# Kernel tuning notes

Measured on AMD Instinct MI355X. Metric: run time of the kernel, lower is better.

## Reference

```python
import jax, jax.numpy as jnp
import numpy as np

DIM = 2048
DIM_HEAD = 64
HEADS = 16
FF_MULT = 4
LORA_R = 8
ATTN_INNER = DIM_HEAD * HEADS            # 1024
FF_INNER = DIM * FF_MULT                 # 8192
FUSED_DIMS = (ATTN_INNER, DIM_HEAD, DIM_HEAD, FF_INNER * 2)
B, N = 2, 2048


def setup_inputs() -> dict:
    key = jax.random.key(0)
    ks = jax.random.split(key, 12)
    s = 0.02
    inp = {
        "x": jax.random.normal(ks[0], (B, N, DIM), dtype=jnp.float32),
        "gamma": jnp.ones((DIM,), dtype=jnp.float32),
        "w_fused": jax.random.normal(ks[1], (DIM, sum(FUSED_DIMS)), dtype=jnp.float32) * s,
        "w_attn_out": jax.random.normal(ks[2], (ATTN_INNER, DIM), dtype=jnp.float32) * s,
        "w_ff_out": jax.random.normal(ks[3], (FF_INNER, DIM), dtype=jnp.float32) * s,
        "lora_q_a": jax.random.normal(ks[4], (DIM, LORA_R), dtype=jnp.float32) * s,
        "lora_q_b": jax.random.normal(ks[5], (LORA_R, ATTN_INNER), dtype=jnp.float32) * s,
        "lora_k_a": jax.random.normal(ks[6], (DIM, LORA_R), dtype=jnp.float32) * s,
        "lora_k_b": jax.random.normal(ks[7], (LORA_R, DIM_HEAD), dtype=jnp.float32) * s,
        "lora_v_a": jax.random.normal(ks[8], (DIM, LORA_R), dtype=jnp.float32) * s,
        "lora_v_b": jax.random.normal(ks[9], (LORA_R, DIM_HEAD), dtype=jnp.float32) * s,
        "lora_o_a": jax.random.normal(ks[10], (ATTN_INNER, LORA_R), dtype=jnp.float32) * s,
        "lora_o_b": jax.random.normal(ks[11], (LORA_R, DIM), dtype=jnp.float32) * s,
    }
    return inp


def _rotate_half(x):
    x1, x2 = jnp.split(x, 2, axis=-1)
    return jnp.concatenate((-x2, x1), axis=-1)


def _rope(pos, t):
    return t * jnp.cos(pos) + _rotate_half(t) * jnp.sin(pos)


def _forward(x, gamma, w_fused, w_attn_out, w_ff_out,
             lora_q_a, lora_q_b, lora_k_a, lora_k_b,
             lora_v_a, lora_v_b, lora_o_a, lora_o_b):
    b, n, d = x.shape
    # LayerNorm (beta = 0)
    mu = jnp.mean(x, axis=-1, keepdims=True)
    var = jnp.var(x, axis=-1, keepdims=True)
    xn = (x - mu) * jax.lax.rsqrt(var + 1e-5) * gamma

    fused = xn @ w_fused
    i0, i1, i2 = np.cumsum(FUSED_DIMS)[:3]
    q, k, v, ff = fused[..., :i0], fused[..., i0:i1], fused[..., i1:i2], fused[..., i2:]

    # LoRA additive terms
    q = q + (xn @ lora_q_a) @ lora_q_b
    k = k + (xn @ lora_k_a) @ lora_k_b
    v = v + (xn @ lora_v_a) @ lora_v_b

    q = q.reshape(b, n, HEADS, DIM_HEAD).transpose(0, 2, 1, 3)  # b h n d
    q = q * (DIM_HEAD ** -0.5)

    # rotary embedding: pos (n, dim_head)
    inv_freq = 1.0 / (10000.0 ** (jnp.arange(0, DIM_HEAD, 2, dtype=jnp.float32) / DIM_HEAD))
    freqs = jnp.arange(n, dtype=jnp.float32)[:, None] * inv_freq[None, :]
    pos = jnp.concatenate((freqs, freqs), axis=-1)
    q = _rope(pos, q)
    k = _rope(pos, k)  # k is b n d (multi-query, single kv head)

    sim = jnp.einsum('bhid,bjd->bhij', q, k)
    causal = jnp.triu(jnp.ones((n, n), dtype=bool), k=1)
    sim = jnp.where(causal, -jnp.finfo(sim.dtype).max, sim)
    attn = jax.nn.softmax(sim, axis=-1)
    out = jnp.einsum('bhij,bjd->bhid', attn, v)
    out = out.transpose(0, 2, 1, 3).reshape(b, n, ATTN_INNER)

    attn_out = out @ w_attn_out + (out @ lora_o_a) @ lora_o_b

    # SwiGLU: chunk -> (x_ff, gate); silu(gate) * x_ff
    x_ff, gate = jnp.split(ff, 2, axis=-1)
    ff_out = (jax.nn.silu(gate) * x_ff) @ w_ff_out

    return attn_out + ff_out


def reference(x, gamma, w_fused, w_attn_out, w_ff_out,
              lora_q_a, lora_q_b, lora_k_a, lora_k_b,
              lora_v_a, lora_v_b, lora_o_a, lora_o_b):
    return _forward(x, gamma, w_fused, w_attn_out, w_ff_out,
                    lora_q_a, lora_q_b, lora_k_a, lora_k_b,
                    lora_v_a, lora_v_b, lora_o_a, lora_o_b)
```

## Files before the change

### kernel.cpp

```cpp
#include <hip/hip_runtime.h>
#include <cstdint>


typedef __bf16 bf16_t;
typedef __bf16 bf16x8 __attribute__((ext_vector_type(8)));
typedef float f32x4 __attribute__((ext_vector_type(4)));

#define LOG2E 1.44269504088896340736f
#define LOG2_10K 13.287712379549449f

#define WAITCNT_VM(N) __builtin_amdgcn_s_waitcnt(0x0F70 | (N))

__device__ __forceinline__ void gload_lds16(const void* g, void* l) {
  __builtin_amdgcn_global_load_lds(
      (__attribute__((address_space(1))) void*)(uintptr_t)g,
      (__attribute__((address_space(3))) void*)(uint32_t)(uintptr_t)l,
      16, 0, 0);
}

__device__ __forceinline__ f32x4 mfma16(bf16x8 a, bf16x8 b, f32x4 c) {
  return __builtin_amdgcn_mfma_f32_16x16x32_bf16(a, b, c, 0, 0, 0);
}

__global__ __launch_bounds__(256) void ln_kernel(
    const float* __restrict__ x, const float* __restrict__ gamma,
    bf16_t* __restrict__ xn)
{
  const int row = blockIdx.x;
  const int t = threadIdx.x;
  const float4* xr = (const float4*)(x + (size_t)row * 2048);
  float4 a = xr[t * 2];
  float4 b = xr[t * 2 + 1];
  float s  = a.x + a.y + a.z + a.w + b.x + b.y + b.z + b.w;
  float ss = a.x*a.x + a.y*a.y + a.z*a.z + a.w*a.w
           + b.x*b.x + b.y*b.y + b.z*b.z + b.w*b.w;
  #pragma unroll
  for (int m = 1; m < 64; m <<= 1) {
    s  += __shfl_xor(s, m);
    ss += __shfl_xor(ss, m);
  }
  __shared__ float red[8];
  const int wave = t >> 6, lane = t & 63;
  if (lane == 0) { red[wave] = s; red[4 + wave] = ss; }
  __syncthreads();
  const float stot  = red[0] + red[1] + red[2] + red[3];
  const float sstot = red[4] + red[5] + red[6] + red[7];
  const float mu  = stot * (1.f / 2048.f);
  const float var = sstot * (1.f / 2048.f) - mu * mu;
  const float rs  = rsqrtf(var + 1e-5f);
  float v[8] = {a.x, a.y, a.z, a.w, b.x, b.y, b.z, b.w};
  bf16x8 o;
  #pragma unroll
  for (int e = 0; e < 8; ++e)
    o[e] = (bf16_t)((v[e] - mu) * rs * gamma[t * 8 + e]);
  *(bf16x8*)(xn + (size_t)row * 2048 + t * 8) = o;
}

__global__ __launch_bounds__(256) void transpose_wf_kernel(
    const float* __restrict__ w,
    const float* __restrict__ qa, const float* __restrict__ qb,
    const float* __restrict__ ka, const float* __restrict__ kb,
    const float* __restrict__ va, const float* __restrict__ vb,
    bf16_t* __restrict__ wfT)
{
  __shared__ float tile[64][65];
  const int t  = threadIdx.x;
  const int n0 = blockIdx.x * 64;
  const int k0 = blockIdx.y * 64;
  #pragma unroll
  for (int it = 0; it < 4; ++it) {
    const int kr = (t >> 4) + it * 16;
    const float4 vv = *(const float4*)(w + (size_t)(k0 + kr) * 17536 + n0 + (t & 15) * 4);
    tile[kr][(t & 15) * 4 + 0] = vv.x;
    tile[kr][(t & 15) * 4 + 1] = vv.y;
    tile[kr][(t & 15) * 4 + 2] = vv.z;
    tile[kr][(t & 15) * 4 + 3] = vv.w;
  }
  __syncthreads();
  const float* la = nullptr; const float* lb = nullptr;
  int nbo = 0, ldlb = 0;
  if (n0 < 1024)      { la = qa; lb = qb; nbo = n0;        ldlb = 1024; }
  else if (n0 < 1088) { la = ka; lb = kb; nbo = n0 - 1024; ldlb = 64;   }
  else if (n0 < 1152) { la = va; lb = vb; nbo = n0 - 1088; ldlb = 64;   }
  #pragma unroll
  for (int it = 0; it < 2; ++it) {
    const int nl = (t >> 3) + it * 32;
    const int kl = (t & 7) * 8;
    float vals[8];
    #pragma unroll
    for (int e = 0; e < 8; ++e) vals[e] = tile[kl + e][nl];
    if (la) {
      float bc[8];
      #pragma unroll
      for (int r = 0; r < 8; ++r) bc[r] = lb[r * ldlb + nbo + nl];
      #pragma unroll
      for (int e = 0; e < 8; ++e) {
        const float* ar = la + (size_t)(k0 + kl + e) * 8;
        float d = 0.f;
        #pragma unroll
        for (int r = 0; r < 8; ++r) d += ar[r] * bc[r];
        vals[e] += d;
      }
    }
    bf16x8 o;
    #pragma unroll
    for (int e = 0; e < 8; ++e) o[e] = (bf16_t)vals[e];
    *(bf16x8*)(wfT + (size_t)(n0 + nl) * 2048 + k0 + kl) = o;
  }
}

__global__ __launch_bounds__(256) void transpose_w2_kernel(
    const float* __restrict__ wff,
    const float* __restrict__ watt,
    const float* __restrict__ oa, const float* __restrict__ ob,
    bf16_t* __restrict__ w2T)
{
  __shared__ float tile[64][65];
  const int t  = threadIdx.x;
  const int n0 = blockIdx.x * 64;
  const int k0 = blockIdx.y * 64;
  const bool isatt = (k0 >= 8192);
  const float* src = isatt ? (watt + (size_t)(k0 - 8192) * 2048)
                           : (wff + (size_t)k0 * 2048);
  #pragma unroll
  for (int it = 0; it < 4; ++it) {
    const int kr = (t >> 4) + it * 16;
    const float4 vv = *(const float4*)(src + (size_t)kr * 2048 + n0 + (t & 15) * 4);
    tile[kr][(t & 15) * 4 + 0] = vv.x;
    tile[kr][(t & 15) * 4 + 1] = vv.y;
    tile[kr][(t & 15) * 4 + 2] = vv.z;
    tile[kr][(t & 15) * 4 + 3] = vv.w;
  }
  __syncthreads();
  #pragma unroll
  for (int it = 0; it < 2; ++it) {
    const int nl = (t >> 3) + it * 32;
    const int kl = (t & 7) * 8;
    float vals[8];
    #pragma unroll
    for (int e = 0; e < 8; ++e) vals[e] = tile[kl + e][nl];
    if (isatt) {
      float bc[8];
      #pragma unroll
      for (int r = 0; r < 8; ++r) bc[r] = ob[r * 2048 + n0 + nl];
      #pragma unroll
      for (int e = 0; e < 8; ++e) {
        const float* ar = oa + (size_t)(k0 - 8192 + kl + e) * 8;
        float d = 0.f;
        #pragma unroll
        for (int r = 0; r < 8; ++r) d += ar[r] * bc[r];
        vals[e] += d;
      }
    }
    bf16x8 o;
    #pragma unroll
    for (int e = 0; e < 8; ++e) o[e] = (bf16_t)vals[e];
    *(bf16x8*)(w2T + (size_t)(n0 + nl) * 9216 + k0 + kl) = o;
  }
}

__device__ __forceinline__ void gemm_core_128x128(
    const bf16_t* __restrict__ A, int ldA, int m0,
    const bf16_t* __restrict__ BT, int ldB, int n0,
    int K, bf16_t* As, bf16_t* Bs, f32x4* acc)
{
  const int t = threadIdx.x;
  const int wave = t >> 6;
  const int lane = t & 63;
  const int quad = lane >> 4;
  const int ln15 = lane & 15;
  const int wm = wave & 1, wn = wave >> 1;

  const bf16_t* gA = A + (size_t)(m0 + (t >> 2)) * ldA + ((t & 3) << 3);
  const bf16_t* gB = BT + (size_t)(n0 + (t >> 2)) * ldB + ((t & 3) << 3);
  char* lA = (char*)As + wave * 1024;
  char* lB = (char*)Bs + wave * 1024;
  const size_t sA64 = (size_t)64 * ldA;
  const size_t sB64 = (size_t)64 * ldB;
  const int aoff = (wm * 64 + ln15) * 32 + quad * 8;
  const int boff = (wn * 64 + ln15) * 32 + quad * 8;

  for (int kt = 0; kt < K; kt += 32) {
    gload_lds16(gA,        lA);
    gload_lds16(gA + sA64, lA + 4096);
    gload_lds16(gB,        lB);
    gload_lds16(gB + sB64, lB + 4096);
    gA += 32;
    gB += 32;
    __syncthreads();
    bf16x8 a0 = *(const bf16x8*)(As + aoff);
    bf16x8 a1 = *(const bf16x8*)(As + aoff + 512);
    bf16x8 a2 = *(const bf16x8*)(As + aoff + 1024);
    bf16x8 a3 = *(const bf16x8*)(As + aoff + 1536);
    bf16x8 b0 = *(const bf16x8*)(Bs + boff);
    bf16x8 b1 = *(const bf16x8*)(Bs + boff + 512);
    bf16x8 b2 = *(const bf16x8*)(Bs + boff + 1024);
    bf16x8 b3 = *(const bf16x8*)(Bs + boff + 1536);
    acc[0]  = mfma16(a0, b0, acc[0]);
    acc[1]  = mfma16(a0, b1, acc[1]);
    acc[2]  = mfma16(a0, b2, acc[2]);
    acc[3]  = mfma16(a0, b3, acc[3]);
    acc[4]  = mfma16(a1, b0, acc[4]);
    acc[5]  = mfma16(a1, b1, acc[5]);
    acc[6]  = mfma16(a1, b2, acc[6]);
    acc[7]  = mfma16(a1, b3, acc[7]);
    acc[8]  = mfma16(a2, b0, acc[8]);
    acc[9]  = mfma16(a2, b1, acc[9]);
    acc[10] = mfma16(a2, b2, acc[10]);
    acc[11] = mfma16(a2, b3, acc[11]);
    acc[12] = mfma16(a3, b0, acc[12]);
    acc[13] = mfma16(a3, b1, acc[13]);
    acc[14] = mfma16(a3, b2, acc[14]);
    acc[15] = mfma16(a3, b3, acc[15]);
    __syncthreads();
  }
}

__device__ __forceinline__ void gemm_core_dual(
    const bf16_t* gA, const bf16_t* gB0, const bf16_t* gB1,
    int ldA, int ldB, int K,
    bf16_t* As, bf16_t* B0s, bf16_t* B1s,
    f32x4* acc0, f32x4* acc1)
{
  const int t = threadIdx.x;
  const int wave = t >> 6;
  const int lane = t & 63;
  const int quad = lane >> 4;
  const int ln15 = lane & 15;
  const int wm = wave & 1, wn = wave >> 1;

  char* lA = (char*)As + wave * 1024;
  char* l0 = (char*)B0s + wave * 1024;
  char* l1 = (char*)B1s + wave * 1024;
  const size_t sA64 = (size_t)64 * ldA;
  const size_t sB64 = (size_t)64 * ldB;
  const int aoff = (wm * 64 + ln15) * 32 + quad * 8;
  const int boff = (wn * 64 + ln15) * 32 + quad * 8;

  for (int kt = 0; kt < K; kt += 32) {
    gload_lds16(gA,         lA);
    gload_lds16(gA + sA64,  lA + 4096);
    gload_lds16(gB0,        l0);
    gload_lds16(gB0 + sB64, l0 + 4096);
    gload_lds16(gB1,        l1);
    gload_lds16(gB1 + sB64, l1 + 4096);
    gA += 32; gB0 += 32; gB1 += 32;
    __syncthreads();
    bf16x8 a0 = *(const bf16x8*)(As + aoff);
    bf16x8 a1 = *(const bf16x8*)(As + aoff + 512);
    bf16x8 a2 = *(const bf16x8*)(As + aoff + 1024);
    bf16x8 a3 = *(const bf16x8*)(As + aoff + 1536);
    bf16x8 p0 = *(const bf16x8*)(B0s + boff);
    bf16x8 p1 = *(const bf16x8*)(B0s + boff + 512);
    bf16x8 p2 = *(const bf16x8*)(B0s + boff + 1024);
    bf16x8 p3 = *(const bf16x8*)(B0s + boff + 1536);
    bf16x8 q0 = *(const bf16x8*)(B1s + boff);
    bf16x8 q1 = *(const bf16x8*)(B1s + boff + 512);
    bf16x8 q2 = *(const bf16x8*)(B1s + boff + 1024);
    bf16x8 q3 = *(const bf16x8*)(B1s + boff + 1536);
    acc0[0]  = mfma16(a0, p0, acc0[0]);
    acc0[1]  = mfma16(a0, p1, acc0[1]);
    acc0[2]  = mfma16(a0, p2, acc0[2]);
    acc0[3]  = mfma16(a0, p3, acc0[3]);
    acc1[0]  = mfma16(a0, q0, acc1[0]);
    acc1[1]  = mfma16(a0, q1, acc1[1]);
    acc1[2]  = mfma16(a0, q2, acc1[2]);
    acc1[3]  = mfma16(a0, q3, acc1[3]);
    acc0[4]  = mfma16(a1, p0, acc0[4]);
    acc0[5]  = mfma16(a1, p1, acc0[5]);
    acc0[6]  = mfma16(a1, p2, acc0[6]);
    acc0[7]  = mfma16(a1, p3, acc0[7]);
    acc1[4]  = mfma16(a1, q0, acc1[4]);
    acc1[5]  = mfma16(a1, q1, acc1[5]);
    acc1[6]  = mfma16(a1, q2, acc1[6]);
    acc1[7]  = mfma16(a1, q3, acc1[7]);
    acc0[8]  = mfma16(a2, p0, acc0[8]);
    acc0[9]  = mfma16(a2, p1, acc0[9]);
    acc0[10] = mfma16(a2, p2, acc0[10]);
    acc0[11] = mfma16(a2, p3, acc0[11]);
    acc1[8]  = mfma16(a2, q0, acc1[8]);
    acc1[9]  = mfma16(a2, q1, acc1[9]);
    acc1[10] = mfma16(a2, q2, acc1[10]);
    acc1[11] = mfma16(a2, q3, acc1[11]);
    acc0[12] = mfma16(a3, p0, acc0[12]);
    acc0[13] = mfma16(a3, p1, acc0[13]);
    acc0[14] = mfma16(a3, p2, acc0[14]);
    acc0[15] = mfma16(a3, p3, acc0[15]);
    acc1[12] = mfma16(a3, q0, acc1[12]);
    acc1[13] = mfma16(a3, q1, acc1[13]);
    acc1[14] = mfma16(a3, q2, acc1[14]);
    acc1[15] = mfma16(a3, q3, acc1[15]);
    __syncthreads();
  }
}

__global__ __launch_bounds__(256, 2) void gemm1_qkv_kernel(
    const bf16_t* __restrict__ xn, const bf16_t* __restrict__ wfT,
    bf16_t* __restrict__ Q, bf16_t* __restrict__ K, bf16_t* __restrict__ Vt)
{
  __shared__ __align__(16) bf16_t As[128 * 32];
  __shared__ __align__(16) bf16_t B0s[128 * 32];
  __shared__ __align__(16) bf16_t B1s[128 * 32];
  const int m0 = blockIdx.x * 128;
  const int y = blockIdx.y;
  const int t = threadIdx.x;
  const int wave = t >> 6, lane = t & 63;
  const int quad = lane >> 4, ln15 = lane & 15;
  const int wm = wave & 1, wn = wave >> 1;

  const int rb = m0 + wm * 64 + quad * 4;
  const float invf0 = exp2f(-(float)ln15 * (LOG2_10K / 32.0f));
  const float invf1 = exp2f(-(float)(16 + ln15) * (LOG2_10K / 32.0f));

  if (y < 4) {
    const bf16_t* gA  = xn  + (size_t)(m0 + (t >> 2)) * 2048 + ((t & 3) << 3);
    const bf16_t* gB0 = wfT + (size_t)(y * 256 + (t >> 2)) * 2048 + ((t & 3) << 3);
    const bf16_t* gB1 = wfT + (size_t)(y * 256 + 128 + (t >> 2)) * 2048 + ((t & 3) << 3);
    f32x4 acc0[16], acc1[16];
    #pragma unroll
    for (int f = 0; f < 16; ++f) {
      acc0[f] = (f32x4){0.f, 0.f, 0.f, 0.f};
      acc1[f] = (f32x4){0.f, 0.f, 0.f, 0.f};
    }
    gemm_core_dual(gA, gB0, gB1, 2048, 2048, 2048, As, B0s, B1s, acc0, acc1);
    #pragma unroll
    for (int half = 0; half < 2; ++half) {
      const f32x4* acc = half ? acc1 : acc0;
      const int hd = y * 4 + half * 2 + wn;
      #pragma unroll
      for (int i = 0; i < 4; ++i) {
        #pragma unroll
        for (int rr = 0; rr < 4; ++rr) {
          const int row = rb + i * 16 + rr;
          const int b = row >> 11, n = row & 2047;
          const float fn = (float)n;
          float s0, c0, s1, c1;
          __sincosf(fn * invf0, &s0, &c0);
          __sincosf(fn * invf1, &s1, &c1);
          float vals[4];
          #pragma unroll
          for (int j = 0; j < 4; ++j) vals[j] = acc[i * 4 + j][rr];
          #pragma unroll
          for (int j = 0; j < 4; ++j) {
            const float rot = (j < 2) ? -vals[j + 2] : vals[j - 2];
            const float c = (j & 1) ? c1 : c0;
            const float s = (j & 1) ? s1 : s0;
            const float o = (vals[j] * c + rot * s) * 0.125f;
            Q[(((size_t)b * 16 + hd) * 2048 + n) * 64 + j * 16 + ln15] = (bf16_t)o;
          }
        }
      }
    }
  } else {
    f32x4 acc[16];
    #pragma unroll
    for (int f = 0; f < 16; ++f) acc[f] = (f32x4){0.f, 0.f, 0.f, 0.f};
    gemm_core_128x128(xn, 2048, m0, wfT, 2048, 1024, 2048, As, B0s, acc);
    const bool is_k = (wn == 0);
    #pragma unroll
    for (int i = 0; i < 4; ++i) {
      #pragma unroll
      for (int rr = 0; rr < 4; ++rr) {
        const int row = rb + i * 16 + rr;
        const int b = row >> 11, n = row & 2047;
        float vals[4];
        #pragma unroll
        for (int j = 0; j < 4; ++j) vals[j] = acc[i * 4 + j][rr];
        if (is_k) {
          const float fn = (float)n;
          float s0, c0, s1, c1;
          __sincosf(fn * invf0, &s0, &c0);
          __sincosf(fn * invf1, &s1, &c1);
          #pragma unroll
          for (int j = 0; j < 4; ++j) {
            const float rot = (j < 2) ? -vals[j + 2] : vals[j - 2];
            const float c = (j & 1) ? c1 : c0;
            const float s = (j & 1) ? s1 : s0;
            K[((size_t)b * 2048 + n) * 64 + j * 16 + ln15] = (bf16_t)(vals[j] * c + rot * s);
          }
        } else {
          #pragma unroll
          for (int j = 0; j < 4; ++j)
            Vt[((size_t)b * 64 + j * 16 + ln15) * 2048 + n] = (bf16_t)vals[j];
        }
      }
    }
  }
}


#define FF_STG() {                                                           \
    char* lA_ = lds + sst + w * 1024;                                        \
    gload_lds16(gA, lA_);                                                    \
    gload_lds16(gA + (size_t)128 * 2048, lA_ + 8192);                        \
    char* lB_ = lds + 65536 + sst + w * 1024;                                \
    gload_lds16(gB0, lB_);                                                   \
    gload_lds16(gB1, lB_ + 8192);                                            \
    gA += 32; gB0 += 32; gB1 += 32;                                          \
    sst = (sst + 16384) & 65535; }

#define FF_RD(DA, DB) {                                                      \
    _Pragma("unroll")                                                        \
    for (int mf_ = 0; mf_ < 8; ++mf_)                                        \
      DA[mf_] = *(const bf16x8*)(lds + srd + wm * 8192 + mf_ * 1024 + ro);   \
    _Pragma("unroll")                                                        \
    for (int nf_ = 0; nf_ < 4; ++nf_)                                        \
      DB[nf_] = *(const bf16x8*)(lds + 65536 + srd + wn * 4096 + nf_ * 1024 + ro); \
    srd = (srd + 16384) & 65535;                                             \
    __builtin_amdgcn_sched_barrier(0); }

#define FF_MM(SA, SB) {                                                      \
    __builtin_amdgcn_s_setprio(1);                                           \
    _Pragma("unroll")                                                        \
    for (int mf_ = 0; mf_ < 8; ++mf_) {                                      \
      _Pragma("unroll")                                                      \
      for (int nf_ = 0; nf_ < 4; ++nf_)                                      \
        acc[mf_][nf_] = mfma16(SA[mf_], SB[nf_], acc[mf_][nf_]);             \
    }                                                                        \
    __builtin_amdgcn_s_setprio(0); }

#define FF_SYNC4() { WAITCNT_VM(4); __builtin_amdgcn_s_barrier(); }

__global__ __launch_bounds__(512, 2) void gemm1_ff_kernel(
    const bf16_t* __restrict__ xn, const bf16_t* __restrict__ wfT,
    bf16_t* __restrict__ A2)
{
  __shared__ __align__(16) char lds[131072];
  const int m0 = blockIdx.x * 256;
  const int c0 = blockIdx.y * 128;
  const int t = threadIdx.x;
  const int w = t >> 6, lane = t & 63;
  const int quad = lane >> 4, ln15 = lane & 15;
  const int wm = w & 1, wn = w >> 1;

  const int p  = w * 64 + lane;
  const int r  = p >> 2;
  const int cl = (p & 3) ^ ((r >> 1) & 3);
  const bf16_t* gA = xn + (size_t)(m0 + r) * 2048 + cl * 8;
  const int r2 = r + 128;
  const int cm0 = c0 + ((r  >> 5) << 4) + (r  & 15);
  const int cm1 = c0 + ((r2 >> 5) << 4) + (r2 & 15);
  const int wr0 = ((r  >> 4) & 1) ? (1152 + cm0) : (9344 + cm0);
  const int wr1 = ((r2 >> 4) & 1) ? (1152 + cm1) : (9344 + cm1);
  const bf16_t* gB0 = wfT + (size_t)wr0 * 2048 + cl * 8;
  const bf16_t* gB1 = wfT + (size_t)wr1 * 2048 + cl * 8;

  const int ro = ln15 * 64 + ((quad ^ ((ln15 >> 1) & 3)) * 16);

  f32x4 acc[8][4];
  #pragma unroll
  for (int mf = 0; mf < 8; ++mf)
    #pragma unroll
    for (int nf = 0; nf < 4; ++nf)
      acc[mf][nf] = (f32x4){0.f, 0.f, 0.f, 0.f};

  int sst = 0, srd = 0;
  #pragma unroll
  for (int pt = 0; pt < 3; ++pt) FF_STG();
  FF_SYNC4();

  bf16x8 fA[8], fB[4], nA[8], nB[4];
  FF_RD(fA, fB);

  for (int i = 0; i < 30; ++i) {
    FF_STG(); FF_RD(nA, nB); FF_MM(fA, fB); FF_SYNC4();
    FF_STG(); FF_RD(fA, fB); FF_MM(nA, nB); FF_SYNC4();
  }
  FF_STG(); FF_RD(nA, nB); FF_MM(fA, fB); FF_SYNC4();
  FF_RD(fA, fB); FF_MM(nA, nB);
  WAITCNT_VM(0);
  __builtin_amdgcn_s_barrier();
  FF_RD(nA, nB); FF_MM(fA, fB);
  FF_MM(nA, nB);

  const int row0 = m0 + wm * 128 + quad * 4;
  const int col0 = c0 + wn * 32 + ln15;
  #pragma unroll
  for (int mf = 0; mf < 8; ++mf)
    #pragma unroll
    for (int rr = 0; rr < 4; ++rr) {
      bf16_t* dst = A2 + (size_t)(row0 + mf * 16 + rr) * 9216 + col0;
      #pragma unroll
      for (int j = 0; j < 2; ++j) {
        const float g  = acc[mf][2 * j][rr];
        const float xv = acc[mf][2 * j + 1][rr];
        dst[j * 16] = (bf16_t)(xv * (g / (1.f + exp2f(-g * LOG2E))));
      }
    }
}

#define G2_STG() {                                                           \
    char* lA_ = lds + sstA + w * 1024;                                       \
    gload_lds16(gA, lA_);                                                    \
    gload_lds16(gA + (size_t)128 * 9216, lA_ + 8192);                        \
    gload_lds16(gB, lds + 65536 + sstB + w * 1024);                          \
    gA += 32; gB += 32;                                                      \
    sstA = (sstA + 16384) & 65535;                                           \
    sstB = (sstB + 8192) & 32767; }

#define G2_RD(DA, DB) {                                                      \
    _Pragma("unroll")                                                        \
    for (int mf_ = 0; mf_ < 4; ++mf_)                                        \
      DA[mf_] = *(const bf16x8*)(lds + srdA + wm * 4096 + mf_ * 1024 + ro);  \
    _Pragma("unroll")                                                        \
    for (int nf_ = 0; nf_ < 4; ++nf_)                                        \
      DB[nf_] = *(const bf16x8*)(lds + 65536 + srdB + wn * 4096 + nf_ * 1024 + ro); \
    srdA = (srdA + 16384) & 65535;                                           \
    srdB = (srdB + 8192) & 32767;                                            \
    __builtin_amdgcn_sched_barrier(0); }

#define G2_MM(SA, SB) {                                                      \
    __builtin_amdgcn_s_setprio(1);                                           \
    _Pragma("unroll")                                                        \
    for (int mf_ = 0; mf_ < 4; ++mf_) {                                      \
      _Pragma("unroll")                                                      \
      for (int nf_ = 0; nf_ < 4; ++nf_)                                      \
        acc[mf_][nf_] = mfma16(SA[mf_], SB[nf_], acc[mf_][nf_]);             \
    }                                                                        \
    __builtin_amdgcn_s_setprio(0); }

#define G2_SYNC3() { WAITCNT_VM(3); __builtin_amdgcn_s_barrier(); }

__global__ __launch_bounds__(512, 2) void gemm2_kernel(
    const bf16_t* __restrict__ A2, const bf16_t* __restrict__ w2T,
    float* __restrict__ out)
{
  __shared__ __align__(16) char lds[98304];
  const int m0 = blockIdx.x * 256;
  const int n0 = blockIdx.y * 128;
  const int t = threadIdx.x;
  const int w = t >> 6, lane = t & 63;
  const int quad = lane >> 4, ln15 = lane & 15;
  const int wm = w & 3, wn = w >> 2;

  const int p  = w * 64 + lane;
  const int r  = p >> 2;
  const int cl = (p & 3) ^ ((r >> 1) & 3);
  const bf16_t* gA = A2  + (size_t)(m0 + r) * 9216 + cl * 8;
  const bf16_t* gB = w2T + (size_t)(n0 + r) * 9216 + cl * 8;

  const int ro = ln15 * 64 + ((quad ^ ((ln15 >> 1) & 3)) * 16);

  f32x4 acc[4][4];
  #pragma unroll
  for (int mf = 0; mf < 4; ++mf)
    #pragma unroll
    for (int nf = 0; nf < 4; ++nf)
      acc[mf][nf] = (f32x4){0.f, 0.f, 0.f, 0.f};

  int sstA = 0, sstB = 0, srdA = 0, srdB = 0;
  #pragma unroll
  for (int pt = 0; pt < 3; ++pt) G2_STG();
  G2_SYNC3();

  bf16x8 fA[4], fB[4], nA[4], nB[4];
  G2_RD(fA, fB);

  for (int i = 0; i < 142; ++i) {
    G2_STG(); G2_RD(nA, nB); G2_MM(fA, fB); G2_SYNC3();
    G2_STG(); G2_RD(fA, fB); G2_MM(nA, nB); G2_SYNC3();
  }
  G2_STG(); G2_RD(nA, nB); G2_MM(fA, fB); G2_SYNC3();
  G2_RD(fA, fB); G2_MM(nA, nB);
  WAITCNT_VM(0);
  __builtin_amdgcn_s_barrier();
  G2_RD(nA, nB); G2_MM(fA, fB);
  G2_MM(nA, nB);

  const int row0 = m0 + wm * 64 + quad * 4;
  const int col0 = n0 + wn * 64 + ln15;
  #pragma unroll
  for (int mf = 0; mf < 4; ++mf)
    #pragma unroll
    for (int rr = 0; rr < 4; ++rr) {
      float* dst = out + (size_t)(row0 + mf * 16 + rr) * 2048 + col0;
      #pragma unroll
      for (int nf = 0; nf < 4; ++nf)
        dst[nf * 16] = acc[mf][nf][rr];
    }
}

__global__ __launch_bounds__(256, 2) void attn_kernel(
    const bf16_t* __restrict__ Q, const bf16_t* __restrict__ Kg_,
    const bf16_t* __restrict__ Vt, bf16_t* __restrict__ A2)
{
  __shared__ __align__(16) bf16_t Qs[64 * 64];
  __shared__ __align__(16) bf16_t Ks[64 * 64];
  __shared__ __align__(16) bf16_t Vs[64 * 64];
  __shared__ __align__(16) bf16_t Ps[64 * 64];
  const int pidx = blockIdx.x, bh = blockIdx.y;
  const int b = bh >> 4, h = bh & 15;
  const int t = threadIdx.x;
  const int wave = t >> 6, lane = t & 63;
  const int quad = lane >> 4, ln15 = lane & 15;

  const bf16_t* Kg = Kg_ + (size_t)b * 2048 * 64;
  const bf16_t* Vg = Vt + (size_t)b * 64 * 2048;

  for (int hlf = 0; hlf < 2; ++hlf) {
    const int qt = hlf ? (31 - pidx) : pidx;
    const int qm0 = qt * 64;
    const bf16_t* Qg = Q + ((size_t)bh * 2048 + qm0) * 64;

    {
      const bf16_t* g = Qg + (size_t)(t >> 3) * 64 + ((t & 7) << 3);
      char* l = (char*)Qs + wave * 1024;
      gload_lds16(g,           l);
      gload_lds16(g + 32 * 64, l + 4096);
    }

    float mstate[4], lstate[4];
    f32x4 o_acc[4];
    #pragma unroll
    for (int rr = 0; rr < 4; ++rr) { mstate[rr] = -1e30f; lstate[rr] = 0.f; }
    #pragma unroll
    for (int jd = 0; jd < 4; ++jd) o_acc[jd] = (f32x4){0.f, 0.f, 0.f, 0.f};

    const int njt = qt + 1;
    for (int jt = 0; jt < njt; ++jt) {
      {
        const bf16_t* kg = Kg + (size_t)(jt * 64 + (t >> 3)) * 64 + ((t & 7) << 3);
        char* lk = (char*)Ks + wave * 1024;
        gload_lds16(kg,           lk);
        gload_lds16(kg + 32 * 64, lk + 4096);
        const bf16_t* vg = Vg + (size_t)(t >> 3) * 2048 + jt * 64 + ((t & 7) << 3);
        char* lv = (char*)Vs + wave * 1024;
        gload_lds16(vg,                   lv);
        gload_lds16(vg + (size_t)32*2048, lv + 4096);
      }
      __syncthreads();

      f32x4 sA[4];
      #pragma unroll
      for (int j = 0; j < 4; ++j) sA[j] = (f32x4){0.f, 0.f, 0.f, 0.f};
      #pragma unroll
      for (int ks = 0; ks < 2; ++ks) {
        bf16x8 aq = *(const bf16x8*)(Qs + (wave * 16 + ln15) * 64 + ks * 32 + quad * 8);
        #pragma unroll
        for (int j = 0; j < 4; ++j) {
          bf16x8 bk = *(const bf16x8*)(Ks + (j * 16 + ln15) * 64 + ks * 32 + quad * 8);
          sA[j] = mfma16(aq, bk, sA[j]);
        }
      }

      const bool needmask = (jt * 64 + 63 > qm0 + wave * 16);
      const int row0 = qm0 + wave * 16 + quad * 4;
      float alpha[4];
      #pragma unroll
      for (int rr = 0; rr < 4; ++rr) {
        const int rowg = row0 + rr;
        if (needmask) {
          #pragma unroll
          for (int j = 0; j < 4; ++j) {
            const int colg = jt * 64 + j * 16 + ln15;
            if (colg > rowg) sA[j][rr] = -1e30f;
          }
        }
        float mx = fmaxf(fmaxf(sA[0][rr], sA[1][rr]),
                         fmaxf(sA[2][rr], sA[3][rr]));
        mx = fmaxf(mx, __shfl_xor(mx, 1));
        mx = fmaxf(mx, __shfl_xor(mx, 2));
        mx = fmaxf(mx, __shfl_xor(mx, 4));
        mx = fmaxf(mx, __shfl_xor(mx, 8));
        const float mold = mstate[rr];
        const float mnew = fmaxf(mold, mx);
        const float al = exp2f((mold - mnew) * LOG2E);
        float rsum = 0.f;
        #pragma unroll
        for (int j = 0; j < 4; ++j) {
          const float p = exp2f((sA[j][rr] - mnew) * LOG2E);
          sA[j][rr] = p;
          rsum += p;
        }
        rsum += __shfl_xor(rsum, 1);
        rsum += __shfl_xor(rsum, 2);
        rsum += __shfl_xor(rsum, 4);
        rsum += __shfl_xor(rsum, 8);
        lstate[rr] = lstate[rr] * al + rsum;
        mstate[rr] = mnew;
        alpha[rr] = al;
      }
      #pragma unroll
      for (int jd = 0; jd < 4; ++jd)
        #pragma unroll
        for (int rr = 0; rr < 4; ++rr)
          o_acc[jd][rr] *= alpha[rr];
      #pragma unroll
      for (int j = 0; j < 4; ++j)
        #pragma unroll
        for (int rr = 0; rr < 4; ++rr)
          Ps[wave * 1024 + (quad * 4 + rr) * 64 + j * 16 + ln15] = (bf16_t)sA[j][rr];

      #pragma unroll
      for (int ks = 0; ks < 2; ++ks) {
        bf16x8 ap = *(const bf16x8*)(Ps + wave * 1024 + ln15 * 64 + ks * 32 + quad * 8);
        #pragma unroll
        for (int jd = 0; jd < 4; ++jd) {
          bf16x8 bv = *(const bf16x8*)(Vs + (jd * 16 + ln15) * 64 + ks * 32 + quad * 8);
          o_acc[jd] = mfma16(ap, bv, o_acc[jd]);
        }
      }
      __syncthreads();
    }

    const int row0 = qm0 + wave * 16 + quad * 4;
    #pragma unroll
    for (int rr = 0; rr < 4; ++rr) {
      const float inv = 1.f / lstate[rr];
      bf16_t* dst = A2 + ((size_t)b * 2048 + row0 + rr) * 9216 + 8192 + h * 64 + ln15;
      #pragma unroll
      for (int jd = 0; jd < 4; ++jd)
        dst[jd * 16] = (bf16_t)(o_acc[jd][rr] * inv);
    }
  }
}

extern "C" void kernel_launch(void* const* d_in, const int* in_sizes, int n_in,
                              void* d_out, int out_size, void* d_ws, size_t ws_size,
                              hipStream_t stream)
{
  const float* x      = (const float*)d_in[0];
  const float* gamma  = (const float*)d_in[1];
  const float* wfused = (const float*)d_in[2];
  const float* watt   = (const float*)d_in[3];
  const float* wff    = (const float*)d_in[4];
  const float* qa     = (const float*)d_in[5];
  const float* qb     = (const float*)d_in[6];
  const float* ka     = (const float*)d_in[7];
  const float* kb     = (const float*)d_in[8];
  const float* va     = (const float*)d_in[9];
  const float* vb     = (const float*)d_in[10];
  const float* oa     = (const float*)d_in[11];
  const float* ob     = (const float*)d_in[12];
  float* out = (float*)d_out;

  char* ws = (char*)d_ws;
  bf16_t* xn  = (bf16_t*)(ws);
  bf16_t* wfT = (bf16_t*)(ws + 16777216);
  bf16_t* w2T = (bf16_t*)(ws + 88604672);
  bf16_t* A2  = (bf16_t*)(ws + 126353408);
  bf16_t* Qr  = (bf16_t*)(ws + 201850880);
  bf16_t* Kr  = (bf16_t*)(ws + 210239488);
  bf16_t* Vtr = (bf16_t*)(ws + 210763776);

  ln_kernel<<<dim3(4096), dim3(256), 0, stream>>>(x, gamma, xn);
  transpose_wf_kernel<<<dim3(274, 32), dim3(256), 0, stream>>>(
      wfused, qa, qb, ka, kb, va, vb, wfT);
  transpose_w2_kernel<<<dim3(32, 144), dim3(256), 0, stream>>>(
      wff, watt, oa, ob, w2T);
  gemm1_qkv_kernel<<<dim3(32, 5), dim3(256), 0, stream>>>(xn, wfT, Qr, Kr, Vtr);
  gemm1_ff_kernel<<<dim3(16, 64), dim3(512), 0, stream>>>(xn, wfT, A2);
  attn_kernel<<<dim3(16, 32), dim3(256), 0, stream>>>(Qr, Kr, Vtr, A2);
  gemm2_kernel<<<dim3(16, 16), dim3(512), 0, stream>>>(A2, w2T, out);
}
```

Measured before the change: 877.1 us.

## Use 256x256 tiles with split-K atomics in gemm2 and split gemm1_ff launch

```diff
diff --git a/kernel.cpp b/kernel.cpp
--- a/kernel.cpp
+++ b/kernel.cpp
@@ -423,10 +423,10 @@
 
 __global__ __launch_bounds__(512, 2) void gemm1_ff_kernel(
     const bf16_t* __restrict__ xn, const bf16_t* __restrict__ wfT,
-    bf16_t* __restrict__ A2)
+    bf16_t* __restrict__ A2, int m_base)
 {
   __shared__ __align__(16) char lds[131072];
-  const int m0 = blockIdx.x * 256;
+  const int m0 = m_base + blockIdx.x * 256;
   const int c0 = blockIdx.y * 128;
   const int t = threadIdx.x;
   const int w = t >> 6, lane = t & 63;
@@ -489,94 +489,75 @@
     }
 }
 
+
 #define G2_STG() {                                                           \
-    char* lA_ = lds + sstA + w * 1024;                                       \
+    char* lA_ = lds + sst + w * 1024;                                        \
     gload_lds16(gA, lA_);                                                    \
     gload_lds16(gA + (size_t)128 * 9216, lA_ + 8192);                        \
-    gload_lds16(gB, lds + 65536 + sstB + w * 1024);                          \
-    gA += 32; gB += 32;                                                      \
-    sstA = (sstA + 16384) & 65535;                                           \
-    sstB = (sstB + 8192) & 32767; }
-
-#define G2_RD(DA, DB) {                                                      \
-    _Pragma("unroll")                                                        \
-    for (int mf_ = 0; mf_ < 4; ++mf_)                                        \
-      DA[mf_] = *(const bf16x8*)(lds + srdA + wm * 4096 + mf_ * 1024 + ro);  \
-    _Pragma("unroll")                                                        \
-    for (int nf_ = 0; nf_ < 4; ++nf_)                                        \
-      DB[nf_] = *(const bf16x8*)(lds + 65536 + srdB + wn * 4096 + nf_ * 1024 + ro); \
-    srdA = (srdA + 16384) & 65535;                                           \
-    srdB = (srdB + 8192) & 32767;                                            \
-    __builtin_amdgcn_sched_barrier(0); }
-
-#define G2_MM(SA, SB) {                                                      \
-    __builtin_amdgcn_s_setprio(1);                                           \
-    _Pragma("unroll")                                                        \
-    for (int mf_ = 0; mf_ < 4; ++mf_) {                                      \
-      _Pragma("unroll")                                                      \
-      for (int nf_ = 0; nf_ < 4; ++nf_)                                      \
-        acc[mf_][nf_] = mfma16(SA[mf_], SB[nf_], acc[mf_][nf_]);             \
-    }                                                                        \
-    __builtin_amdgcn_s_setprio(0); }
-
-#define G2_SYNC3() { WAITCNT_VM(3); __builtin_amdgcn_s_barrier(); }
+    char* lB_ = lds + 65536 + sst + w * 1024;                                \
+    gload_lds16(gB0, lB_);                                                   \
+    gload_lds16(gB1, lB_ + 8192);                                            \
+    gA += 32; gB0 += 32; gB1 += 32;                                          \
+    sst = (sst + 16384) & 65535; }
 
 __global__ __launch_bounds__(512, 2) void gemm2_kernel(
     const bf16_t* __restrict__ A2, const bf16_t* __restrict__ w2T,
     float* __restrict__ out)
 {
-  __shared__ __align__(16) char lds[98304];
+  __shared__ __align__(16) char lds[131072];
   const int m0 = blockIdx.x * 256;
-  const int n0 = blockIdx.y * 128;
+  const int n0 = blockIdx.y * 256;
+  const int k0 = blockIdx.z * 4608;
   const int t = threadIdx.x;
   const int w = t >> 6, lane = t & 63;
   const int quad = lane >> 4, ln15 = lane & 15;
-  const int wm = w & 3, wn = w >> 2;
+  const int wm = w & 1, wn = w >> 1;
 
   const int p  = w * 64 + lane;
   const int r  = p >> 2;
   const int cl = (p & 3) ^ ((r >> 1) & 3);
-  const bf16_t* gA = A2  + (size_t)(m0 + r) * 9216 + cl * 8;
-  const bf16_t* gB = w2T + (size_t)(n0 + r) * 9216 + cl * 8;
+  const bf16_t* gA  = A2  + (size_t)(m0 + r) * 9216 + k0 + cl * 8;
+  const bf16_t* gB0 = w2T + (size_t)(n0 + r) * 9216 + k0 + cl * 8;
+  const bf16_t* gB1 = w2T + (size_t)(n0 + 128 + r) * 9216 + k0 + cl * 8;
 
   const int ro = ln15 * 64 + ((quad ^ ((ln15 >> 1) & 3)) * 16);
 
-  f32x4 acc[4][4];
-  #pragma unroll
-  for (int mf = 0; mf < 4; ++mf)
+  f32x4 acc[8][4];
+  #pragma unroll
+  for (int mf = 0; mf < 8; ++mf)
     #pragma unroll
     for (int nf = 0; nf < 4; ++nf)
       acc[mf][nf] = (f32x4){0.f, 0.f, 0.f, 0.f};
 
-  int sstA = 0, sstB = 0, srdA = 0, srdB = 0;
+  int sst = 0, srd = 0;
   #pragma unroll
   for (int pt = 0; pt < 3; ++pt) G2_STG();
-  G2_SYNC3();
-
-  bf16x8 fA[4], fB[4], nA[4], nB[4];
-  G2_RD(fA, fB);
-
-  for (int i = 0; i < 142; ++i) {
-    G2_STG(); G2_RD(nA, nB); G2_MM(fA, fB); G2_SYNC3();
-    G2_STG(); G2_RD(fA, fB); G2_MM(nA, nB); G2_SYNC3();
-  }
-  G2_STG(); G2_RD(nA, nB); G2_MM(fA, fB); G2_SYNC3();
-  G2_RD(fA, fB); G2_MM(nA, nB);
+  FF_SYNC4();
+
+  bf16x8 fA[8], fB[4], nA[8], nB[4];
+  FF_RD(fA, fB);
+
+  for (int i = 0; i < 70; ++i) {
+    G2_STG(); FF_RD(nA, nB); FF_MM(fA, fB); FF_SYNC4();
+    G2_STG(); FF_RD(fA, fB); FF_MM(nA, nB); FF_SYNC4();
+  }
+  G2_STG(); FF_RD(nA, nB); FF_MM(fA, fB); FF_SYNC4();
+  FF_RD(fA, fB); FF_MM(nA, nB);
   WAITCNT_VM(0);
   __builtin_amdgcn_s_barrier();
-  G2_RD(nA, nB); G2_MM(fA, fB);
-  G2_MM(nA, nB);
-
-  const int row0 = m0 + wm * 64 + quad * 4;
+  FF_RD(nA, nB); FF_MM(fA, fB);
+  FF_MM(nA, nB);
+
+  const int row0 = m0 + wm * 128 + quad * 4;
   const int col0 = n0 + wn * 64 + ln15;
   #pragma unroll
-  for (int mf = 0; mf < 4; ++mf)
+  for (int mf = 0; mf < 8; ++mf)
     #pragma unroll
     for (int rr = 0; rr < 4; ++rr) {
       float* dst = out + (size_t)(row0 + mf * 16 + rr) * 2048 + col0;
       #pragma unroll
       for (int nf = 0; nf < 4; ++nf)
-        dst[nf * 16] = acc[mf][nf][rr];
+        unsafeAtomicAdd(dst + nf * 16, acc[mf][nf][rr]);
     }
 }
 
@@ -743,13 +724,16 @@
   bf16_t* Kr  = (bf16_t*)(ws + 210239488);
   bf16_t* Vtr = (bf16_t*)(ws + 210763776);
 
+  hipMemsetAsync(d_out, 0, (size_t)out_size * sizeof(float), stream);
+
   ln_kernel<<<dim3(4096), dim3(256), 0, stream>>>(x, gamma, xn);
   transpose_wf_kernel<<<dim3(274, 32), dim3(256), 0, stream>>>(
       wfused, qa, qb, ka, kb, va, vb, wfT);
   transpose_w2_kernel<<<dim3(32, 144), dim3(256), 0, stream>>>(
       wff, watt, oa, ob, w2T);
   gemm1_qkv_kernel<<<dim3(32, 5), dim3(256), 0, stream>>>(xn, wfT, Qr, Kr, Vtr);
-  gemm1_ff_kernel<<<dim3(16, 64), dim3(512), 0, stream>>>(xn, wfT, A2);
+  gemm1_ff_kernel<<<dim3(8, 64), dim3(512), 0, stream>>>(xn, wfT, A2, 0);
+  gemm1_ff_kernel<<<dim3(8, 64), dim3(512), 0, stream>>>(xn, wfT, A2, 2048);
   attn_kernel<<<dim3(16, 32), dim3(256), 0, stream>>>(Qr, Kr, Vtr, A2);
-  gemm2_kernel<<<dim3(16, 16), dim3(512), 0, stream>>>(A2, w2T, out);
-}
+  gemm2_kernel<<<dim3(16, 8, 2), dim3(512), 0, stream>>>(A2, w2T, out);
+}
```

Measured after the change: 906.4 us. 1.03x slower.
